# Kernel tuning notes

Measured on AMD Instinct MI355X. Metric: run time of the kernel, lower is better.

## Reference

```python
import jax, jax.numpy as jnp
import numpy as np

N_NODES = 100000
N_EDGES = 1000000
IN_FEATS = 64
HID = 128
NUM_CLASSES = 10


def setup_inputs() -> dict:
    key = jax.random.key(0)
    ks = jax.random.split(key, 8)
    x = jax.random.normal(ks[0], (N_NODES, IN_FEATS), dtype=jnp.float32)
    edge_index = jax.random.randint(ks[1], (2, N_EDGES), 0, N_NODES, dtype=jnp.int64)
    # Glorot-style init scale for weights
    def w(k, fan_in, fan_out):
        s = (2.0 / (fan_in + fan_out)) ** 0.5
        return jax.random.normal(k, (fan_in, fan_out), dtype=jnp.float32) * s
    return {
        "x": x,
        "edge_index": edge_index,
        "W1": w(ks[2], IN_FEATS, HID),
        "b1": jnp.zeros((HID,), dtype=jnp.float32),
        "W2": w(ks[3], HID, HID),
        "b2": jnp.zeros((HID,), dtype=jnp.float32),
        "Wl": w(ks[4], HID, NUM_CLASSES),
        "bl": jnp.zeros((NUM_CLASSES,), dtype=jnp.float32),
    }


def _gcn_conv(x, src, dst, norm, W, b, num_nodes):
    # PyG GCNConv: h = x W, then out_i = sum_{j->i} norm_ij * h_j + b
    h = x @ W  # [N, out]
    msgs = h[src] * norm[:, None]  # gather + scale  [E+N, out]
    out = jax.ops.segment_sum(msgs, dst, num_segments=num_nodes)
    return out + b


def reference(x, edge_index, W1, b1, W2, b2, Wl, bl):
    N = x.shape[0]
    loops = jnp.arange(N, dtype=edge_index.dtype)
    src = jnp.concatenate([edge_index[0], loops])  # source nodes (messages from)
    dst = jnp.concatenate([edge_index[1], loops])  # target nodes (aggregate at)
    # symmetric normalization: deg over targets (includes self-loops)
    deg = jax.ops.segment_sum(jnp.ones(dst.shape, dtype=x.dtype), dst, num_segments=N)
    dinv = jnp.where(deg > 0, jax.lax.rsqrt(deg), 0.0)
    norm = dinv[src] * dinv[dst]  # [E+N]

    h = jax.nn.relu(_gcn_conv(x, src, dst, norm, W1, b1, N))
    h = jax.nn.relu(_gcn_conv(h, src, dst, norm, W2, b2, N))
    return jax.nn.log_softmax(h @ Wl + bl, axis=1)
```

## Files before the change

kernel.cpp:

```cpp
#include <hip/hip_runtime.h>
#include <hip/hip_fp16.h>
#include <math.h>

#define NUM_CLASSES 10

#define BSH 7
#define BSZ 128
#define BCAP 1792
#define NBMAX 1024
#define P1BATCH 4096
#define PREPB 97

typedef _Float16 half8  __attribute__((ext_vector_type(8)));
typedef _Float16 half4t __attribute__((ext_vector_type(4)));
typedef float    floatx4 __attribute__((ext_vector_type(4)));

__global__ __launch_bounds__(256) void prep_p1_kernel(const float* __restrict__ W1,
                                                      const float* __restrict__ W2,
                                                      const float* __restrict__ Wlc,
                                                      _Float16* __restrict__ W1t,
                                                      _Float16* __restrict__ W2t,
                                                      _Float16* __restrict__ Wct,
                                                      const int* __restrict__ src,
                                                      const int* __restrict__ dst,
                                                      int* __restrict__ bucket_fill,
                                                      unsigned* __restrict__ pairs, int E) {
    __shared__ int hist[NBMAX], base[NBMAX], cur[NBMAX];
    const int tid = threadIdx.x;
    const int b = blockIdx.x;

    if (b < PREPB) {
        if (b < 32) {
            int i = b * 256 + tid;
            int k = i >> 7, c = i & 127;
            W1t[c * 72 + k] = (_Float16)W1[i];
        } else if (b < 96) {
            int i = (b - 32) * 256 + tid;
            int k = i >> 7, c = i & 127;
            W2t[c * 136 + k] = (_Float16)W2[i];
        } else {
            for (int i = tid; i < 16 * 136; i += 256) {
                int c = i / 136, k = i - c * 136;
                float v = (c < NUM_CLASSES && k < 128) ? Wlc[k * NUM_CLASSES + c] : 0.0f;
                Wct[i] = (_Float16)v;
            }
        }
        return;
    }

    for (int i = tid; i < NBMAX; i += 256) { hist[i] = 0; cur[i] = 0; }
    __syncthreads();
    const int bb = (b - PREPB) * P1BATCH;
    unsigned pk[16];
    int bk[16];
    int cnt = 0;
#pragma unroll
    for (int i = 0; i < 16; ++i) {
        int idx = bb + i * 256 + tid;
        if (idx < E) {
            int s = src[idx], d = dst[idx];
            bk[i] = d >> BSH;
            pk[i] = ((unsigned)s << BSH) | (unsigned)(d & (BSZ - 1));
            atomicAdd(&hist[bk[i]], 1);
            cnt = i + 1;
        }
    }
    __syncthreads();
    for (int i = tid; i < NBMAX; i += 256)
        if (hist[i] > 0) base[i] = atomicAdd(&bucket_fill[i], hist[i]);
    __syncthreads();
#pragma unroll
    for (int i = 0; i < 16; ++i) {
        if (i < cnt) {
            int bi = bk[i];
            int r = atomicAdd(&cur[bi], 1) + base[bi];
            if (r < BCAP) pairs[(size_t)bi * BCAP + r] = pk[i];
        }
    }
}

__global__ __launch_bounds__(256) void csr_p2_kernel(const int* __restrict__ bucket_fill,
                                                     const unsigned* __restrict__ pairs,
                                                     const float* __restrict__ x,
                                                     int* __restrict__ rowstart,
                                                     float* __restrict__ dinv,
                                                     int* __restrict__ csr_src,
                                                     __half2* __restrict__ xs_h,
                                                     int N, int nbuck) {
    __shared__ int cnt[BSZ], excl[BSZ], cur[BSZ];
    __shared__ int s1[256];
    const int tid = threadIdx.x;
    const int b = blockIdx.x;
    const int node0 = b << BSH;
    const int nodes_b = min(BSZ, N - node0);

    if (tid < BSZ) { cnt[tid] = 0; cur[tid] = 0; }
    int part = 0;
    for (int j = tid; j < b; j += 256) part += bucket_fill[j];
    s1[tid] = part;
    __syncthreads();
    for (int off = 128; off > 0; off >>= 1) {
        if (tid < off) s1[tid] += s1[tid + off];
        __syncthreads();
    }
    const int bbase = s1[0];
    const int ne = bucket_fill[b];
    __syncthreads();

    const unsigned* bp = pairs + (size_t)b * BCAP;
    for (int i = tid; i < ne; i += 256)
        atomicAdd(&cnt[bp[i] & (BSZ - 1)], 1);
    __syncthreads();
    int c = (tid < BSZ) ? cnt[tid] : 0;
    if (tid < BSZ) s1[tid] = c;
    __syncthreads();
    for (int off = 1; off < BSZ; off <<= 1) {
        int t = (tid < BSZ && tid >= off) ? s1[tid - off] : 0;
        __syncthreads();
        if (tid < BSZ) s1[tid] += t;
        __syncthreads();
    }
    if (tid < BSZ) excl[tid] = s1[tid] - c;
    __syncthreads();

    if (tid < nodes_b) {
        rowstart[node0 + tid] = bbase + excl[tid];
        dinv[node0 + tid] = rsqrtf((float)cnt[tid] + 1.0f);
    }
    if (b == nbuck - 1 && tid == 0) rowstart[N] = bbase + ne;

    for (int i = tid; i < nodes_b * 32; i += 256) {
        int ln = i >> 5;
        float d = rsqrtf((float)cnt[ln] + 1.0f);
        float2 v = ((const float2*)x)[(size_t)node0 * 32 + i];
        xs_h[(size_t)node0 * 32 + i] = __floats2half2_rn(v.x * d, v.y * d);
    }
    for (int i = tid; i < ne; i += 256) {
        unsigned p = bp[i];
        int d = (int)(p & (BSZ - 1));
        int r = atomicAdd(&cur[d], 1);
        csr_src[bbase + excl[d] + r] = (int)(p >> BSH);
    }
}

__global__ __launch_bounds__(256) void gather64_kernel(const __half2* __restrict__ xs,
                                                       const float* __restrict__ dinv,
                                                       const int* __restrict__ rowstart,
                                                       const int* __restrict__ csr_src,
                                                       __half2* __restrict__ out, int N) {
    int node = (blockIdx.x * 256 + threadIdx.x) >> 6;
    int lane = threadIdx.x & 63;
    if (node >= N) return;
    int f2 = lane & 31;

    int beg = rowstart[node];
    int end = rowstart[node + 1];
    int deg = end - beg;

    float2 self = __half22float2(xs[(size_t)node * 32 + f2]);
    float2 acc;

    if (deg <= 16) {
        int myidx = (lane < deg) ? csr_src[beg + lane] : node;
        float comp = (float)(deg - 15);
        acc.x = self.x * comp;
        acc.y = self.y * comp;
        float2 v[16];
#pragma unroll
        for (int u = 0; u < 16; ++u) {
            int s = __shfl(myidx, u);
            v[u] = __half22float2(xs[(size_t)s * 32 + f2]);
        }
#pragma unroll
        for (int u = 0; u < 16; ++u) { acc.x += v[u].x; acc.y += v[u].y; }
    } else {
        int lim = deg < 64 ? deg : 64;
        int myidx = (lane < lim) ? csr_src[beg + lane] : node;
        int itersUp = (lim + 7) & ~7;
        float comp = (float)(1 - (itersUp - lim));
        acc.x = self.x * comp;
        acc.y = self.y * comp;
        for (int j = 0; j < itersUp; j += 8) {
            int s[8];
#pragma unroll
            for (int u = 0; u < 8; ++u) s[u] = __shfl(myidx, j + u);
            float2 v[8];
#pragma unroll
            for (int u = 0; u < 8; ++u) v[u] = __half22float2(xs[(size_t)s[u] * 32 + f2]);
#pragma unroll
            for (int u = 0; u < 8; ++u) { acc.x += v[u].x; acc.y += v[u].y; }
        }
        for (int j = beg + 64; j < end; ++j) {
            float2 v = __half22float2(xs[(size_t)csr_src[j] * 32 + f2]);
            acc.x += v.x;
            acc.y += v.y;
        }
    }
    if (lane < 32) {
        float d = dinv[node];
        out[(size_t)node * 32 + f2] = __floats2half2_rn(d * acc.x, d * acc.y);
    }
}

template <int K, bool SCALE_OUT>
__global__ __launch_bounds__(256) void gemm_mfma_kernel(const _Float16* __restrict__ In,
                                                        const _Float16* __restrict__ Wt,
                                                        const float* __restrict__ bias,
                                                        const float* __restrict__ dinv,
                                                        _Float16* __restrict__ Out, int N) {
    constexpr int KP = K + 8;
    constexpr int NC = K / 32;
    __shared__ _Float16 Wl[128 * KP];
    __shared__ float bias_s[128];
    const int tid = threadIdx.x;

    for (int i = tid; i < (128 * KP) / 8; i += 256)
        ((floatx4*)Wl)[i] = ((const floatx4*)Wt)[i];
    if (tid < 128) bias_s[tid] = bias[tid];
    __syncthreads();

    const int lane = tid & 63;
    const int wave = tid >> 6;
    const int q = lane >> 4;
    const int l15 = lane & 15;

#pragma unroll
    for (int iter = 0; iter < 2; ++iter) {
        int myrow = blockIdx.x * 128 + iter * 64 + wave * 16 + l15;
        int r = myrow < N ? myrow : N - 1;
        half8 xf[NC];
#pragma unroll
        for (int c = 0; c < NC; ++c)
            xf[c] = *(const half8*)(In + (size_t)r * K + c * 32 + q * 8);
        floatx4 acc[8];
#pragma unroll
        for (int t = 0; t < 8; ++t) acc[t] = (floatx4){0.f, 0.f, 0.f, 0.f};
#pragma unroll
        for (int c = 0; c < NC; ++c) {
#pragma unroll
            for (int t = 0; t < 8; ++t) {
                half8 wf = *(const half8*)(Wl + (t * 16 + l15) * KP + c * 32 + q * 8);
                acc[t] = __builtin_amdgcn_mfma_f32_16x16x32_f16(wf, xf[c], acc[t], 0, 0, 0);
            }
        }
        if (myrow < N) {
            float sc = SCALE_OUT ? dinv[myrow] : 1.0f;
#pragma unroll
            for (int t = 0; t < 8; ++t) {
                int c0 = t * 16 + q * 4;
                floatx4 bv = *(const floatx4*)&bias_s[c0];
                half4t hh;
#pragma unroll
                for (int j = 0; j < 4; ++j)
                    hh[j] = (_Float16)(sc * fmaxf(acc[t][j] + bv[j], 0.0f));
                *(half4t*)(Out + (size_t)myrow * 128 + c0) = hh;
            }
        }
    }
}

__global__ __launch_bounds__(256) void gather_gemm_final_kernel(
        const __half2* __restrict__ hs,
        const float* __restrict__ dinv,
        const int* __restrict__ rowstart,
        const int* __restrict__ csr_src,
        const _Float16* __restrict__ Wt,
        const float* __restrict__ bias,
        const _Float16* __restrict__ Wct,
        const float* __restrict__ bl,
        float* __restrict__ out, int N) {
    constexpr int KP = 136;
    __shared__ _Float16 As[16 * KP];
    __shared__ _Float16 H2[16 * KP];
    const int tid = threadIdx.x;
    const int lane = tid & 63;
    const int wave = tid >> 6;

    for (int nn = 0; nn < 4; ++nn) {
        const int r = wave * 4 + nn;
        const int node = blockIdx.x * 16 + r;
        if (node < N) {
            int beg = rowstart[node];
            int end = rowstart[node + 1];
            int deg = end - beg;

            float2 self = __half22float2(hs[(size_t)node * 64 + lane]);
            int lim = deg < 64 ? deg : 64;
            int myidx = (lane < lim) ? csr_src[beg + lane] : node;
            int itersUp = (lim + 7) & ~7;
            float comp = (float)(1 - (itersUp - lim));
            float2 acc;
            acc.x = self.x * comp;
            acc.y = self.y * comp;

            for (int j = 0; j < itersUp; j += 8) {
                int s[8];
#pragma unroll
                for (int u = 0; u < 8; ++u) s[u] = __shfl(myidx, j + u);
                float2 v[8];
#pragma unroll
                for (int u = 0; u < 8; ++u) v[u] = __half22float2(hs[(size_t)s[u] * 64 + lane]);
#pragma unroll
                for (int u = 0; u < 8; ++u) { acc.x += v[u].x; acc.y += v[u].y; }
            }
            for (int j = beg + 64; j < end; ++j) {
                float2 v = __half22float2(hs[(size_t)csr_src[j] * 64 + lane]);
                acc.x += v.x;
                acc.y += v.y;
            }
            float d = dinv[node];
            ((__half2*)As)[r * 68 + lane] = __floats2half2_rn(d * acc.x, d * acc.y);
        }
    }
    __syncthreads();

    const int q = lane >> 4;
    const int l15 = lane & 15;

    half8 xf[4];
#pragma unroll
    for (int c = 0; c < 4; ++c)
        xf[c] = *(const half8*)(As + l15 * KP + c * 32 + q * 8);

#pragma unroll
    for (int tt = 0; tt < 2; ++tt) {
        const int t = wave * 2 + tt;
        floatx4 acc = (floatx4){0.f, 0.f, 0.f, 0.f};
#pragma unroll
        for (int c = 0; c < 4; ++c) {
            half8 wf = *(const half8*)(Wt + (t * 16 + l15) * KP + c * 32 + q * 8);
            acc = __builtin_amdgcn_mfma_f32_16x16x32_f16(wf, xf[c], acc, 0, 0, 0);
        }
        const int c0 = t * 16 + q * 4;
        floatx4 bv = *(const floatx4*)(bias + c0);
        half4t hh;
#pragma unroll
        for (int j = 0; j < 4; ++j)
            hh[j] = (_Float16)fmaxf(acc[j] + bv[j], 0.0f);
        *(half4t*)&H2[l15 * KP + c0] = hh;
    }
    __syncthreads();

    if (wave == 0) {
        floatx4 lg = (floatx4){0.f, 0.f, 0.f, 0.f};
#pragma unroll
        for (int c = 0; c < 4; ++c) {
            half8 wcf = *(const half8*)(Wct + l15 * KP + c * 32 + q * 8);
            half8 af = *(const half8*)(H2 + l15 * KP + c * 32 + q * 8);
            lg = __builtin_amdgcn_mfma_f32_16x16x32_f16(wcf, af, lg, 0, 0, 0);
        }
        const int myrow = blockIdx.x * 16 + l15;
        if (myrow < N) {
            float v[4];
#pragma unroll
            for (int reg = 0; reg < 4; ++reg) {
                int cls = q * 4 + reg;
                v[reg] = lg[reg] + ((cls < NUM_CLASSES) ? bl[cls] : -1e30f);
            }
            float mx = fmaxf(fmaxf(v[0], v[1]), fmaxf(v[2], v[3]));
            mx = fmaxf(mx, __shfl_xor(mx, 16));
            mx = fmaxf(mx, __shfl_xor(mx, 32));
            float sm = expf(v[0] - mx) + expf(v[1] - mx) + expf(v[2] - mx) + expf(v[3] - mx);
            sm += __shfl_xor(sm, 16);
            sm += __shfl_xor(sm, 32);
            float lse = mx + logf(sm);
#pragma unroll
            for (int reg = 0; reg < 4; ++reg) {
                int cls = q * 4 + reg;
                if (cls < NUM_CLASSES)
                    out[(size_t)myrow * NUM_CLASSES + cls] = v[reg] - lse;
            }
        }
    }
}

extern "C" void kernel_launch(void* const* d_in, const int* in_sizes, int n_in,
                              void* d_out, int out_size, void* d_ws, size_t ws_size,
                              hipStream_t stream) {
    const float* x  = (const float*)d_in[0];
    const int*   ei = (const int*)d_in[1];
    const float* W1 = (const float*)d_in[2];
    const float* b1 = (const float*)d_in[3];
    const float* W2 = (const float*)d_in[4];
    const float* b2 = (const float*)d_in[5];
    const float* Wlc = (const float*)d_in[6];
    const float* bl = (const float*)d_in[7];
    float* out = (float*)d_out;

    const int N = in_sizes[0] / 64;
    const int E = in_sizes[1] / 2;
    const int* src = ei;
    const int* dst = ei + E;
    const int nbuck = (N + BSZ - 1) >> BSH;

    char* ws = (char*)d_ws;
    int*      bucket_fill = (int*)(ws + 0);
    int*      rowstart    = (int*)(ws + 4096);
    float*    dinv        = (float*)(ws + 524288);
    _Float16* W1t         = (_Float16*)(ws + 1048576);
    _Float16* W2t         = (_Float16*)(ws + 1069056);
    _Float16* Wct         = (_Float16*)(ws + 1103872);
    unsigned* pairs       = (unsigned*)(ws + 2097152);
    int*      csr_src     = (int*)(ws + 12582912);
    __half2*  xs_h        = (__half2*)(ws + 16777216);
    __half2*  g1h         = (__half2*)(ws + 33554432);
    __half2*  a1_h        = (__half2*)(ws + 73400320);

    const int P1B = (E + P1BATCH - 1) / P1BATCH;
    const int GB  = (N + 127) / 128;
    const int WVB = (N + 3) / 4;
    const int FGB = (N + 15) / 16;

    hipMemsetAsync(bucket_fill, 0, nbuck * sizeof(int), stream);
    prep_p1_kernel<<<PREPB + P1B, 256, 0, stream>>>(W1, W2, Wlc, W1t, W2t, Wct,
                                                    src, dst, bucket_fill, pairs, E);
    csr_p2_kernel<<<nbuck, 256, 0, stream>>>(bucket_fill, pairs, x, rowstart, dinv,
                                             csr_src, xs_h, N, nbuck);

    gather64_kernel<<<WVB, 256, 0, stream>>>(xs_h, dinv, rowstart, csr_src, g1h, N);
    gemm_mfma_kernel<64, true><<<GB, 256, 0, stream>>>((const _Float16*)g1h, W1t, b1, dinv,
                                                       (_Float16*)a1_h, N);

    gather_gemm_final_kernel<<<FGB, 256, 0, stream>>>(a1_h, dinv, rowstart, csr_src,
                                                      W2t, b2, Wct, bl, out, N);
}
```

Measured before the change: 218.2 us.

## Fuse layer-1 gather with its MFMA GEMM and preload weights into registers

```diff
diff --git a/kernel.cpp b/kernel.cpp
--- a/kernel.cpp
+++ b/kernel.cpp
@@ -143,118 +143,108 @@
     }
 }
 
-__global__ __launch_bounds__(256) void gather64_kernel(const __half2* __restrict__ xs,
-                                                       const float* __restrict__ dinv,
-                                                       const int* __restrict__ rowstart,
-                                                       const int* __restrict__ csr_src,
-                                                       __half2* __restrict__ out, int N) {
-    int node = (blockIdx.x * 256 + threadIdx.x) >> 6;
-    int lane = threadIdx.x & 63;
-    if (node >= N) return;
-    int f2 = lane & 31;
-
-    int beg = rowstart[node];
-    int end = rowstart[node + 1];
-    int deg = end - beg;
-
-    float2 self = __half22float2(xs[(size_t)node * 32 + f2]);
-    float2 acc;
-
-    if (deg <= 16) {
-        int myidx = (lane < deg) ? csr_src[beg + lane] : node;
-        float comp = (float)(deg - 15);
-        acc.x = self.x * comp;
-        acc.y = self.y * comp;
-        float2 v[16];
-#pragma unroll
-        for (int u = 0; u < 16; ++u) {
-            int s = __shfl(myidx, u);
-            v[u] = __half22float2(xs[(size_t)s * 32 + f2]);
-        }
-#pragma unroll
-        for (int u = 0; u < 16; ++u) { acc.x += v[u].x; acc.y += v[u].y; }
-    } else {
-        int lim = deg < 64 ? deg : 64;
-        int myidx = (lane < lim) ? csr_src[beg + lane] : node;
-        int itersUp = (lim + 7) & ~7;
-        float comp = (float)(1 - (itersUp - lim));
-        acc.x = self.x * comp;
-        acc.y = self.y * comp;
-        for (int j = 0; j < itersUp; j += 8) {
-            int s[8];
-#pragma unroll
-            for (int u = 0; u < 8; ++u) s[u] = __shfl(myidx, j + u);
-            float2 v[8];
-#pragma unroll
-            for (int u = 0; u < 8; ++u) v[u] = __half22float2(xs[(size_t)s[u] * 32 + f2]);
-#pragma unroll
-            for (int u = 0; u < 8; ++u) { acc.x += v[u].x; acc.y += v[u].y; }
-        }
-        for (int j = beg + 64; j < end; ++j) {
-            float2 v = __half22float2(xs[(size_t)csr_src[j] * 32 + f2]);
-            acc.x += v.x;
-            acc.y += v.y;
-        }
-    }
-    if (lane < 32) {
-        float d = dinv[node];
-        out[(size_t)node * 32 + f2] = __floats2half2_rn(d * acc.x, d * acc.y);
-    }
-}
-
-template <int K, bool SCALE_OUT>
-__global__ __launch_bounds__(256) void gemm_mfma_kernel(const _Float16* __restrict__ In,
-                                                        const _Float16* __restrict__ Wt,
-                                                        const float* __restrict__ bias,
-                                                        const float* __restrict__ dinv,
-                                                        _Float16* __restrict__ Out, int N) {
-    constexpr int KP = K + 8;
-    constexpr int NC = K / 32;
-    __shared__ _Float16 Wl[128 * KP];
-    __shared__ float bias_s[128];
+__global__ __launch_bounds__(256) void gather_gemm1_kernel(
+        const __half2* __restrict__ xs,
+        const float* __restrict__ dinv,
+        const int* __restrict__ rowstart,
+        const int* __restrict__ csr_src,
+        const _Float16* __restrict__ Wt,
+        const float* __restrict__ bias,
+        _Float16* __restrict__ Out, int N) {
+    constexpr int KP = 72;
+    __shared__ _Float16 As[16 * KP];
     const int tid = threadIdx.x;
-
-    for (int i = tid; i < (128 * KP) / 8; i += 256)
-        ((floatx4*)Wl)[i] = ((const floatx4*)Wt)[i];
-    if (tid < 128) bias_s[tid] = bias[tid];
-    __syncthreads();
-
     const int lane = tid & 63;
     const int wave = tid >> 6;
     const int q = lane >> 4;
     const int l15 = lane & 15;
 
-#pragma unroll
-    for (int iter = 0; iter < 2; ++iter) {
-        int myrow = blockIdx.x * 128 + iter * 64 + wave * 16 + l15;
-        int r = myrow < N ? myrow : N - 1;
-        half8 xf[NC];
-#pragma unroll
-        for (int c = 0; c < NC; ++c)
-            xf[c] = *(const half8*)(In + (size_t)r * K + c * 32 + q * 8);
-        floatx4 acc[8];
-#pragma unroll
-        for (int t = 0; t < 8; ++t) acc[t] = (floatx4){0.f, 0.f, 0.f, 0.f};
-#pragma unroll
-        for (int c = 0; c < NC; ++c) {
-#pragma unroll
-            for (int t = 0; t < 8; ++t) {
-                half8 wf = *(const half8*)(Wl + (t * 16 + l15) * KP + c * 32 + q * 8);
-                acc[t] = __builtin_amdgcn_mfma_f32_16x16x32_f16(wf, xf[c], acc[t], 0, 0, 0);
-            }
-        }
+    half8 wfr[2][2];
+    floatx4 bvr[2];
+#pragma unroll
+    for (int tt = 0; tt < 2; ++tt) {
+        const int t = wave * 2 + tt;
+#pragma unroll
+        for (int c = 0; c < 2; ++c)
+            wfr[tt][c] = *(const half8*)(Wt + (t * 16 + l15) * KP + c * 32 + q * 8);
+        bvr[tt] = *(const floatx4*)(bias + t * 16 + q * 4);
+    }
+
+    const int f2 = lane & 31;
+    for (int nn = 0; nn < 4; ++nn) {
+        const int r = wave * 4 + nn;
+        const int node = blockIdx.x * 16 + r;
+        if (node < N) {
+            int beg = rowstart[node];
+            int end = rowstart[node + 1];
+            int deg = end - beg;
+
+            float2 self = __half22float2(xs[(size_t)node * 32 + f2]);
+            float2 acc;
+
+            if (deg <= 16) {
+                int myidx = (lane < deg) ? csr_src[beg + lane] : node;
+                float comp = (float)(deg - 15);
+                acc.x = self.x * comp;
+                acc.y = self.y * comp;
+                float2 v[16];
+#pragma unroll
+                for (int u = 0; u < 16; ++u) {
+                    int s = __shfl(myidx, u);
+                    v[u] = __half22float2(xs[(size_t)s * 32 + f2]);
+                }
+#pragma unroll
+                for (int u = 0; u < 16; ++u) { acc.x += v[u].x; acc.y += v[u].y; }
+            } else {
+                int lim = deg < 64 ? deg : 64;
+                int myidx = (lane < lim) ? csr_src[beg + lane] : node;
+                int itersUp = (lim + 7) & ~7;
+                float comp = (float)(1 - (itersUp - lim));
+                acc.x = self.x * comp;
+                acc.y = self.y * comp;
+                for (int j = 0; j < itersUp; j += 8) {
+                    int s[8];
+#pragma unroll
+                    for (int u = 0; u < 8; ++u) s[u] = __shfl(myidx, j + u);
+                    float2 v[8];
+#pragma unroll
+                    for (int u = 0; u < 8; ++u) v[u] = __half22float2(xs[(size_t)s[u] * 32 + f2]);
+#pragma unroll
+                    for (int u = 0; u < 8; ++u) { acc.x += v[u].x; acc.y += v[u].y; }
+                }
+                for (int j = beg + 64; j < end; ++j) {
+                    float2 v = __half22float2(xs[(size_t)csr_src[j] * 32 + f2]);
+                    acc.x += v.x;
+                    acc.y += v.y;
+                }
+            }
+            if (lane < 32) {
+                float d = dinv[node];
+                ((__half2*)As)[r * 36 + f2] = __floats2half2_rn(d * acc.x, d * acc.y);
+            }
+        }
+    }
+    __syncthreads();
+
+    half8 xf[2];
+#pragma unroll
+    for (int c = 0; c < 2; ++c)
+        xf[c] = *(const half8*)(As + l15 * KP + c * 32 + q * 8);
+    const int myrow = blockIdx.x * 16 + l15;
+    float sc = (myrow < N) ? dinv[myrow] : 0.0f;
+#pragma unroll
+    for (int tt = 0; tt < 2; ++tt) {
+        floatx4 acc = (floatx4){0.f, 0.f, 0.f, 0.f};
+#pragma unroll
+        for (int c = 0; c < 2; ++c)
+            acc = __builtin_amdgcn_mfma_f32_16x16x32_f16(wfr[tt][c], xf[c], acc, 0, 0, 0);
         if (myrow < N) {
-            float sc = SCALE_OUT ? dinv[myrow] : 1.0f;
-#pragma unroll
-            for (int t = 0; t < 8; ++t) {
-                int c0 = t * 16 + q * 4;
-                floatx4 bv = *(const floatx4*)&bias_s[c0];
-                half4t hh;
-#pragma unroll
-                for (int j = 0; j < 4; ++j)
-                    hh[j] = (_Float16)(sc * fmaxf(acc[t][j] + bv[j], 0.0f));
-                *(half4t*)(Out + (size_t)myrow * 128 + c0) = hh;
-            }
+            const int c0 = (wave * 2 + tt) * 16 + q * 4;
+            half4t hh;
+#pragma unroll
+            for (int j = 0; j < 4; ++j)
+                hh[j] = (_Float16)(sc * fmaxf(acc[j] + bvr[tt][j], 0.0f));
+            *(half4t*)(Out + (size_t)myrow * 128 + c0) = hh;
         }
     }
 }
@@ -275,6 +265,19 @@
     const int tid = threadIdx.x;
     const int lane = tid & 63;
     const int wave = tid >> 6;
+    const int q = lane >> 4;
+    const int l15 = lane & 15;
+
+    half8 wfr[2][4];
+    floatx4 bvr[2];
+#pragma unroll
+    for (int tt = 0; tt < 2; ++tt) {
+        const int t = wave * 2 + tt;
+#pragma unroll
+        for (int c = 0; c < 4; ++c)
+            wfr[tt][c] = *(const half8*)(Wt + (t * 16 + l15) * KP + c * 32 + q * 8);
+        bvr[tt] = *(const floatx4*)(bias + t * 16 + q * 4);
+    }
 
     for (int nn = 0; nn < 4; ++nn) {
         const int r = wave * 4 + nn;
@@ -314,9 +317,6 @@
     }
     __syncthreads();
 
-    const int q = lane >> 4;
-    const int l15 = lane & 15;
-
     half8 xf[4];
 #pragma unroll
     for (int c = 0; c < 4; ++c)
@@ -327,16 +327,13 @@
         const int t = wave * 2 + tt;
         floatx4 acc = (floatx4){0.f, 0.f, 0.f, 0.f};
 #pragma unroll
-        for (int c = 0; c < 4; ++c) {
-            half8 wf = *(const half8*)(Wt + (t * 16 + l15) * KP + c * 32 + q * 8);
-            acc = __builtin_amdgcn_mfma_f32_16x16x32_f16(wf, xf[c], acc, 0, 0, 0);
-        }
+        for (int c = 0; c < 4; ++c)
+            acc = __builtin_amdgcn_mfma_f32_16x16x32_f16(wfr[tt][c], xf[c], acc, 0, 0, 0);
         const int c0 = t * 16 + q * 4;
-        floatx4 bv = *(const floatx4*)(bias + c0);
         half4t hh;
 #pragma unroll
         for (int j = 0; j < 4; ++j)
-            hh[j] = (_Float16)fmaxf(acc[j] + bv[j], 0.0f);
+            hh[j] = (_Float16)fmaxf(acc[j] + bvr[tt][j], 0.0f);
         *(half4t*)&H2[l15 * KP + c0] = hh;
     }
     __syncthreads();
@@ -403,12 +400,9 @@
     unsigned* pairs       = (unsigned*)(ws + 2097152);
     int*      csr_src     = (int*)(ws + 12582912);
     __half2*  xs_h        = (__half2*)(ws + 16777216);
-    __half2*  g1h         = (__half2*)(ws + 33554432);
     __half2*  a1_h        = (__half2*)(ws + 73400320);
 
     const int P1B = (E + P1BATCH - 1) / P1BATCH;
-    const int GB  = (N + 127) / 128;
-    const int WVB = (N + 3) / 4;
     const int FGB = (N + 15) / 16;
 
     hipMemsetAsync(bucket_fill, 0, nbuck * sizeof(int), stream);
@@ -417,9 +411,8 @@
     csr_p2_kernel<<<nbuck, 256, 0, stream>>>(bucket_fill, pairs, x, rowstart, dinv,
                                              csr_src, xs_h, N, nbuck);
 
-    gather64_kernel<<<WVB, 256, 0, stream>>>(xs_h, dinv, rowstart, csr_src, g1h, N);
-    gemm_mfma_kernel<64, true><<<GB, 256, 0, stream>>>((const _Float16*)g1h, W1t, b1, dinv,
-                                                       (_Float16*)a1_h, N);
+    gather_gemm1_kernel<<<FGB, 256, 0, stream>>>(xs_h, dinv, rowstart, csr_src,
+                                                 W1t, b1, (_Float16*)a1_h, N);
 
     gather_gemm_final_kernel<<<FGB, 256, 0, stream>>>(a1_h, dinv, rowstart, csr_src,
                                                       W2t, b2, Wct, bl, out, N);
```

Result: slower. 225.1 us (+3.2%).
